# Kernel optimization log

Hardware: AMD Instinct MI355X
Metric: run time of the kernel (lower is better)

The kernel has to match this reference:

```python
import jax, jax.numpy as jnp
import numpy as np

V, D, H, L, F, S, B = 32000, 1024, 16, 6, 4096, 2048, 2
HD = D // H
EPS = 1e-5


def _pos_encoding(seq_len, d_model):
    pos = jnp.arange(seq_len, dtype=jnp.float32)[:, None]
    div = jnp.exp(jnp.arange(0, d_model, 2, dtype=jnp.float32) * (-np.log(10000.0) / d_model))
    pe = jnp.zeros((seq_len, d_model), dtype=jnp.float32)
    pe = pe.at[:, 0::2].set(jnp.sin(pos * div))
    pe = pe.at[:, 1::2].set(jnp.cos(pos * div))
    return pe


def setup_inputs() -> dict:
    key = jax.random.key(0)
    ks = jax.random.split(key, 16)
    tokens = jax.random.randint(ks[0], (B, S), 0, V, dtype=jnp.int64)
    mask = jnp.ones((B, 1, 1, S), dtype=jnp.int32)
    emb = jax.random.normal(ks[1], (V, D), dtype=jnp.float32) * 0.02
    sa = 1.0 / np.sqrt(D)
    sf = 1.0 / np.sqrt(F)
    return {
        "tokens": tokens,
        "mask": mask,
        "emb": emb,
        "Wq": jax.random.normal(ks[2], (L, D, D), dtype=jnp.float32) * sa,
        "bq": jnp.zeros((L, D), dtype=jnp.float32),
        "Wk": jax.random.normal(ks[3], (L, D, D), dtype=jnp.float32) * sa,
        "bk": jnp.zeros((L, D), dtype=jnp.float32),
        "Wv": jax.random.normal(ks[4], (L, D, D), dtype=jnp.float32) * sa,
        "bv": jnp.zeros((L, D), dtype=jnp.float32),
        "Wo": jax.random.normal(ks[5], (L, D, D), dtype=jnp.float32) * sa,
        "bo": jnp.zeros((L, D), dtype=jnp.float32),
        "W1": jax.random.normal(ks[6], (L, D, F), dtype=jnp.float32) * sa,
        "b1": jnp.zeros((L, F), dtype=jnp.float32),
        "W2": jax.random.normal(ks[7], (L, F, D), dtype=jnp.float32) * sf,
        "b2": jnp.zeros((L, D), dtype=jnp.float32),
        "g1": jnp.ones((L, D), dtype=jnp.float32),
        "be1": jnp.zeros((L, D), dtype=jnp.float32),
        "g2": jnp.ones((L, D), dtype=jnp.float32),
        "be2": jnp.zeros((L, D), dtype=jnp.float32),
    }


def _layer_norm(x, g, b):
    m = jnp.mean(x, axis=-1, keepdims=True)
    v = jnp.mean(jnp.square(x - m), axis=-1, keepdims=True)
    return (x - m) * jax.lax.rsqrt(v + EPS) * g + b


def _encoder_stack(x, mask, params):
    scale = 1.0 / np.sqrt(HD)

    def layer(x, p):
        Wq, bq, Wk, bk, Wv, bv, Wo, bo, W1, b1, W2, b2, g1, be1, g2, be2 = p
        b, s, d = x.shape
        q = (x @ Wq + bq).reshape(b, s, H, HD).transpose(0, 2, 1, 3)  # [B,H,S,HD]
        k = (x @ Wk + bk).reshape(b, s, H, HD).transpose(0, 2, 1, 3)
        v = (x @ Wv + bv).reshape(b, s, H, HD).transpose(0, 2, 1, 3)
        scores = jnp.einsum("bhqd,bhkd->bhqk", q, k) * scale
        scores = jnp.where(mask == 0, -1e9, scores)
        attn = jax.nn.softmax(scores, axis=-1)
        ctx = jnp.einsum("bhqk,bhkd->bhqd", attn, v)
        attn_out = ctx.transpose(0, 2, 1, 3).reshape(b, s, d) @ Wo + bo
        x = _layer_norm(x + attn_out, g1, be1)
        ff = jax.nn.relu(x @ W1 + b1) @ W2 + b2
        x = _layer_norm(x + ff, g2, be2)
        return x, None

    x, _ = jax.lax.scan(layer, x, params)
    return x


def reference(tokens, mask, emb, Wq, bq, Wk, bk, Wv, bv, Wo, bo, W1, b1, W2, b2, g1, be1, g2, be2):
    x = emb[tokens] + _pos_encoding(tokens.shape[1], emb.shape[1])[None]
    params = (Wq, bq, Wk, bk, Wv, bv, Wo, bo, W1, b1, W2, b2, g1, be1, g2, be2)
    return _encoder_stack(x, mask, params)
```

## Files before the change

### kernel.cpp

```cpp
#include <hip/hip_runtime.h>
#include <hip/hip_bf16.h>
#include <cstdint>
#include <cstddef>


typedef __bf16 bf16;
typedef __bf16 bf16x2 __attribute__((ext_vector_type(2)));
typedef __bf16 bf16x4 __attribute__((ext_vector_type(4)));
typedef __bf16 bf16x8 __attribute__((ext_vector_type(8)));
typedef float  f32x4  __attribute__((ext_vector_type(4)));

#define MFMA16(a, b, c) __builtin_amdgcn_mfma_f32_16x16x32_bf16((a), (b), (c), 0, 0, 0)

static __device__ __forceinline__ void load_lds16(const void* g, void* l) {
  __builtin_amdgcn_global_load_lds((const __attribute__((address_space(1))) void*)g,
                                   (__attribute__((address_space(3))) void*)l, 16, 0, 0);
}

#define BAR()   __builtin_amdgcn_s_barrier()
#define SCH0()  __builtin_amdgcn_sched_barrier(0)
#define VMCNT8() asm volatile("s_waitcnt vmcnt(8)" ::: "memory")
#define VMCNT0() asm volatile("s_waitcnt vmcnt(0)" ::: "memory")

__global__ __launch_bounds__(256) void embed_kernel(const int* __restrict__ tok,
                                                    const float* __restrict__ emb,
                                                    bf16* __restrict__ xo) {
  const int row = blockIdx.x;
  const int s = row & 2047;
  const int t = tok[row];
  const int d0 = threadIdx.x * 4;
  const float4 e = *(const float4*)&emb[(size_t)t * 1024 + d0];
  const float* ef = (const float*)&e;
  bf16x4 o4;
#pragma unroll
  for (int j = 0; j < 4; ++j) {
    const int d = d0 + j;
    const float div = __expf(-(float)(d & ~1) * 0.00899447301950864f);
    const float arg = (float)s * div;
    const float pe = (d & 1) ? cosf(arg) : sinf(arg);
    o4[j] = (bf16)(ef[j] + pe);
  }
  *(bf16x4*)&xo[(size_t)row * 1024 + d0] = o4;
}

struct TJob { const float* src; bf16* dst; int K; int N; int t0; };
struct TArgs { TJob j[6]; };

__global__ __launch_bounds__(256) void wtrans_kernel(TArgs a) {
  __shared__ float t[32][33];
  const int blk = blockIdx.x;
  const float* src = a.j[0].src; bf16* dst = a.j[0].dst;
  int K = a.j[0].K, N = a.j[0].N, t0 = a.j[0].t0;
#pragma unroll
  for (int q = 1; q < 6; ++q)
    if (blk >= a.j[q].t0) { src = a.j[q].src; dst = a.j[q].dst; K = a.j[q].K; N = a.j[q].N; t0 = a.j[q].t0; }
  const int tj = blk - t0;
  const int tilesK = K >> 5;
  const int tk = (tj % tilesK) << 5;
  const int tn = (tj / tilesK) << 5;
  const int lx = threadIdx.x & 31, ly = threadIdx.x >> 5;
#pragma unroll
  for (int i = 0; i < 4; ++i)
    t[ly + 8 * i][lx] = src[(size_t)(tk + ly + 8 * i) * N + tn + lx];
  __syncthreads();
#pragma unroll
  for (int i = 0; i < 4; ++i)
    dst[(size_t)(tn + ly + 8 * i) * K + tk + lx] = (bf16)t[lx][ly + 8 * i];
}

__global__ __launch_bounds__(256) void vtrans_kernel(const bf16* __restrict__ v,
                                                     bf16* __restrict__ vt) {
  __shared__ bf16 t[64][72];
  const int bh = blockIdx.y;
  const int s0 = blockIdx.x * 64;
  const int tid = threadIdx.x;
#pragma unroll
  for (int it = 0; it < 2; ++it) {
    const int idx = tid + it * 256;
    const int sr = idx >> 3, h8 = (idx & 7) * 8;
    *(bf16x8*)&t[sr][h8] = *(const bf16x8*)&v[((size_t)bh * 2048 + s0 + sr) * 64 + h8];
  }
  __syncthreads();
#pragma unroll
  for (int it = 0; it < 2; ++it) {
    const int idx = tid + it * 256;
    const int hd = idx >> 3, s8 = (idx & 7) * 8;
    bf16x8 o;
#pragma unroll
    for (int j = 0; j < 8; ++j) o[j] = t[s8 + j][hd];
    *(bf16x8*)&vt[((size_t)bh * 64 + hd) * 2048 + s0 + s8] = o;
  }
}

static __device__ __forceinline__ bf16x8 ldsfrag(const bf16* base, int row, int colb) {
  int off = row * 128 + colb;
  off ^= ((off >> 7) & 7) << 4;
  return *(const bf16x8*)((const char*)base + off);
}

static __device__ __forceinline__ void stage_tile(const bf16* __restrict__ Ag,
    const bf16* __restrict__ Bg, int Kstr, int kt, bf16* lA, bf16* lB, int tid) {
  const char* wbaseA = (const char*)lA + ((tid >> 6) << 10);
  const char* wbaseB = (const char*)lB + ((tid >> 6) << 10);
#pragma unroll
  for (int s = 0; s < 4; ++s) {
    const int L = s * 8192 + tid * 16;
    const int off = L ^ (((L >> 7) & 7) << 4);
    load_lds16(Ag + (size_t)(off >> 7) * Kstr + kt * 64 + ((off & 127) >> 1),
               (void*)(wbaseA + s * 8192));
  }
#pragma unroll
  for (int s = 0; s < 4; ++s) {
    const int L = s * 8192 + tid * 16;
    const int off = L ^ (((L >> 7) & 7) << 4);
    load_lds16(Bg + (size_t)(off >> 7) * Kstr + kt * 64 + ((off & 127) >> 1),
               (void*)(wbaseB + s * 8192));
  }
}

static __device__ __forceinline__ void compute_tile(const bf16* lA, const bf16* lB,
    int wm, int wn, int lr, int lg, f32x4 (&acc)[8][4]) {
  bf16x8 bfr[4][2];
#pragma unroll
  for (int n = 0; n < 4; ++n)
#pragma unroll
    for (int kk = 0; kk < 2; ++kk)
      bfr[n][kk] = ldsfrag(lB, wn * 64 + n * 16 + lr, kk * 64 + lg * 16);
#pragma unroll
  for (int m = 0; m < 8; ++m) {
    const bf16x8 a0 = ldsfrag(lA, wm * 128 + m * 16 + lr, lg * 16);
    const bf16x8 a1 = ldsfrag(lA, wm * 128 + m * 16 + lr, 64 + lg * 16);
    __builtin_amdgcn_s_setprio(1);
#pragma unroll
    for (int n = 0; n < 4; ++n) {
      acc[m][n] = MFMA16(a0, bfr[n][0], acc[m][n]);
      acc[m][n] = MFMA16(a1, bfr[n][1], acc[m][n]);
    }
    __builtin_amdgcn_s_setprio(0);
  }
}

template <int EPI>
__global__ __launch_bounds__(512, 2) void gemm256(
    const bf16* __restrict__ A, const bf16* __restrict__ Bt,
    int Kstr, int Kloop, int Nn, int nbx,
    const float* __restrict__ bias0, const float* __restrict__ bias1,
    const float* __restrict__ bias2, bf16* __restrict__ outb,
    float* __restrict__ pout,
    bf16* __restrict__ q_out, bf16* __restrict__ k_out, bf16* __restrict__ v_out) {
  __shared__ __align__(16) bf16 lds[4][16384];
  const int bz = blockIdx.y;
  const bf16* Abase = A + (size_t)bz * Kloop;
  const bf16* Bbase = Bt + (size_t)bz * Kloop;
  const int cpx = gridDim.x >> 3;
  const int wg = (blockIdx.x & 7) * cpx + (blockIdx.x >> 3);
  const int bx = wg % nbx, by = wg / nbx;
  const int tid = threadIdx.x;
  const int lane = tid & 63, wave = tid >> 6;
  const int lr = lane & 15, lg = lane >> 4;
  const int wm = wave >> 2, wn = wave & 3;
  const int m0 = by * 256, n0 = bx * 256;

  const bf16* Ag = Abase + (size_t)m0 * Kstr;
  const bf16* Bg = Bbase + (size_t)n0 * Kstr;
  bf16* LA0 = lds[0]; bf16* LB0 = lds[1];
  bf16* LA1 = lds[2]; bf16* LB1 = lds[3];

  f32x4 acc[8][4] = {};
  const int T = Kloop >> 6;

  stage_tile(Ag, Bg, Kstr, 0, LA0, LB0, tid);
  stage_tile(Ag, Bg, Kstr, 1, LA1, LB1, tid);
  VMCNT8(); BAR(); SCH0();

  for (int t = 0; t + 3 < T; t += 2) {
    compute_tile(LA0, LB0, wm, wn, lr, lg, acc);
    BAR(); SCH0();
    stage_tile(Ag, Bg, Kstr, t + 2, LA0, LB0, tid);
    VMCNT8(); BAR(); SCH0();
    compute_tile(LA1, LB1, wm, wn, lr, lg, acc);
    BAR(); SCH0();
    stage_tile(Ag, Bg, Kstr, t + 3, LA1, LB1, tid);
    VMCNT8(); BAR(); SCH0();
  }
  compute_tile(LA0, LB0, wm, wn, lr, lg, acc);
  VMCNT0(); BAR(); SCH0();
  compute_tile(LA1, LB1, wm, wn, lr, lg, acc);

#pragma unroll
  for (int m = 0; m < 8; ++m)
#pragma unroll
    for (int n = 0; n < 4; ++n)
#pragma unroll
      for (int r = 0; r < 4; ++r) {
        const int row = m0 + wm * 128 + m * 16 + lg * 4 + r;
        const int col = n0 + wn * 64 + n * 16 + lr;
        float val = acc[m][n][r];
        if (EPI == 0) {
          const int which = col >> 10, hc = col & 1023;
          const float* bs = (which == 0) ? bias0 : (which == 1) ? bias1 : bias2;
          bf16* dst = (which == 0) ? q_out : (which == 1) ? k_out : v_out;
          val += bs[hc];
          const int b = row >> 11, s = row & 2047;
          const int h = hc >> 6, hd = hc & 63;
          dst[(((size_t)b * 16 + h) * 2048 + s) * 64 + hd] = (bf16)val;
        } else if (EPI == 1) {
          pout[(size_t)bz * 4096 * 1024 + (size_t)row * 1024 + col] = val;
        } else {
          val += bias0[col];
          outb[(size_t)row * Nn + col] = (bf16)(val > 0.f ? val : 0.f);
        }
      }
}

__global__ __launch_bounds__(256) void gemm_sk(
    const bf16* __restrict__ A, const bf16* __restrict__ Bt,
    int Kstride, int Kloop, int nbx, float* __restrict__ pout) {
  __shared__ __align__(16) bf16 As[128 * 32];
  __shared__ __align__(16) bf16 Bs[128 * 32];
  const int bz = blockIdx.y;
  const bf16* Ab = A + (size_t)bz * Kloop;
  const bf16* Bb = Bt + (size_t)bz * Kloop;
  float* pb = pout + (size_t)bz * 4096 * 1024;
  const int cpx = gridDim.x >> 3;
  const int wg = (blockIdx.x & 7) * cpx + (blockIdx.x >> 3);
  const int bx = wg % nbx, by = wg / nbx;
  const int tid = threadIdx.x;
  const int lane = tid & 63;
  const int wave = tid >> 6;
  const int lr = lane & 15, lg = lane >> 4;
  const int m0 = by * 128;
  const int n0 = bx * 128;
  const int wr = (wave >> 1) * 64, wc = (wave & 1) * 64;

  f32x4 acc[4][4] = {};

  const int idx0 = tid, idx1 = tid + 256;
  const char* gA0 = (const char*)(Ab + (size_t)(m0 + (idx0 >> 2)) * Kstride) + (idx0 & 3) * 16;
  const char* gA1 = (const char*)(Ab + (size_t)(m0 + (idx1 >> 2)) * Kstride) + (idx1 & 3) * 16;
  const char* gB0 = (const char*)(Bb + (size_t)(n0 + (idx0 >> 2)) * Kstride) + (idx0 & 3) * 16;
  const char* gB1 = (const char*)(Bb + (size_t)(n0 + (idx1 >> 2)) * Kstride) + (idx1 & 3) * 16;
  bf16* lA0 = &As[(wave * 64) * 8];
  bf16* lA1 = &As[(256 + wave * 64) * 8];
  bf16* lB0 = &Bs[(wave * 64) * 8];
  bf16* lB1 = &Bs[(256 + wave * 64) * 8];

  const int ksteps = Kloop >> 5;
  for (int kt = 0; kt < ksteps; ++kt) {
    load_lds16(gA0, lA0); load_lds16(gA1, lA1);
    load_lds16(gB0, lB0); load_lds16(gB1, lB1);
    gA0 += 64; gA1 += 64; gB0 += 64; gB1 += 64;
    __syncthreads();
    bf16x8 af[2], bfr[2];
    bf16x8 af2[2], bfr2[2];
#pragma unroll
    for (int i = 0; i < 4; ++i) {
      bf16x8 a = *(const bf16x8*)&As[(wr + i * 16 + lr) * 32 + lg * 8];
      if (i < 2) af[i] = a; else af2[i - 2] = a;
    }
#pragma unroll
    for (int j = 0; j < 4; ++j) {
      bf16x8 b = *(const bf16x8*)&Bs[(wc + j * 16 + lr) * 32 + lg * 8];
      if (j < 2) bfr[j] = b; else bfr2[j - 2] = b;
    }
#pragma unroll
    for (int i = 0; i < 4; ++i)
#pragma unroll
      for (int j = 0; j < 4; ++j) {
        const bf16x8 a = (i < 2) ? af[i & 1] : af2[i & 1];
        const bf16x8 b = (j < 2) ? bfr[j & 1] : bfr2[j & 1];
        acc[i][j] = MFMA16(a, b, acc[i][j]);
      }
    __syncthreads();
  }

#pragma unroll
  for (int i = 0; i < 4; ++i)
#pragma unroll
    for (int j = 0; j < 4; ++j)
#pragma unroll
      for (int r = 0; r < 4; ++r) {
        const int row = m0 + wr + i * 16 + lg * 4 + r;
        const int col = n0 + wc + j * 16 + lr;
        pb[(size_t)row * 1024 + col] = acc[i][j][r];
      }
}

__global__ __launch_bounds__(512) void attn_kernel(const bf16* __restrict__ q,
                                                   const bf16* __restrict__ k,
                                                   const bf16* __restrict__ vt,
                                                   bf16* __restrict__ ctxo) {
  __shared__ __align__(16) bf16 Kl[64][64];
  __shared__ __align__(16) bf16 Vt[64][64];
  __shared__ __align__(16) bf16 Pl[8][16][64];
  const int tid = threadIdx.x;
  const int lane = tid & 63, w = tid >> 6;
  const int lr = lane & 15, lg = lane >> 4;
  const int swz = lr & 7;
  const int bh = blockIdx.y;
  const int q0 = blockIdx.x * 128;

  const bf16* qp = q + ((size_t)bh * 2048 + q0 + w * 16) * 64;
  bf16x8 qf0 = *(const bf16x8*)&qp[lr * 64 + lg * 8];
  bf16x8 qf1 = *(const bf16x8*)&qp[lr * 64 + lg * 8 + 32];
  const float qs = 0.18033688011112042f;
#pragma unroll
  for (int j = 0; j < 8; ++j) {
    qf0[j] = (bf16)((float)qf0[j] * qs);
    qf1[j] = (bf16)((float)qf1[j] * qs);
  }
  bf16x8 ones8;
#pragma unroll
  for (int j = 0; j < 8; ++j) ones8[j] = (bf16)1.0f;

  const bf16* kbase = k + (size_t)bh * 2048 * 64;
  const bf16* vtb = vt + (size_t)bh * 64 * 2048;

  const int sr0 = tid >> 3;
  const int c0 = (tid & 7) * 8;
  const int cs0 = c0 ^ ((sr0 & 7) << 3);

  f32x4 acc[4] = {};
  f32x4 accl = {};
  float mq = -1e30f;

  bf16x8 kr[2], vr[2];
  kr[0] = *(const bf16x8*)&kbase[(size_t)sr0 * 64 + c0];
  vr[0] = *(const bf16x8*)&vtb[(size_t)sr0 * 2048 + c0];

#pragma unroll 2
  for (int c = 0; c < 32; ++c) {
    const int pp = c & 1;
    *(bf16x8*)&Kl[sr0][cs0] = kr[pp];
    *(bf16x8*)&Vt[sr0][cs0] = vr[pp];
    if (c + 1 < 32) {
      const int key0n = (c + 1) * 64;
      kr[pp ^ 1] = *(const bf16x8*)&kbase[(size_t)(key0n + sr0) * 64 + c0];
      vr[pp ^ 1] = *(const bf16x8*)&vtb[(size_t)sr0 * 2048 + key0n + c0];
    }
    __syncthreads();

    f32x4 st[4];
    __builtin_amdgcn_s_setprio(1);
#pragma unroll
    for (int ks = 0; ks < 4; ++ks) {
      const bf16x8 kf0 = *(const bf16x8*)&Kl[ks * 16 + lr][(lg ^ swz) << 3];
      const bf16x8 kf1 = *(const bf16x8*)&Kl[ks * 16 + lr][((lg + 4) ^ swz) << 3];
      f32x4 sa = {};
      sa = MFMA16(kf0, qf0, sa);
      sa = MFMA16(kf1, qf1, sa);
      st[ks] = sa;
    }
    __builtin_amdgcn_s_setprio(0);

    float mx = st[0][0];
#pragma unroll
    for (int ks = 0; ks < 4; ++ks)
#pragma unroll
      for (int r = 0; r < 4; ++r) mx = fmaxf(mx, st[ks][r]);
    mx = fmaxf(mx, __shfl_xor(mx, 16));
    mx = fmaxf(mx, __shfl_xor(mx, 32));
    if (!__all(mx - mq <= 8.0f)) {
      const float resc = exp2f(mq - mx);
      mq = mx;
      float rq[4];
#pragma unroll
      for (int r = 0; r < 4; ++r) rq[r] = __shfl(resc, lg * 4 + r);
#pragma unroll
      for (int r = 0; r < 4; ++r) {
        accl[r] *= rq[r];
#pragma unroll
        for (int jn = 0; jn < 4; ++jn) acc[jn][r] *= rq[r];
      }
    }
#pragma unroll
    for (int ks = 0; ks < 4; ++ks) {
      bf16x4 pk;
#pragma unroll
      for (int r = 0; r < 4; ++r) pk[r] = (bf16)exp2f(st[ks][r] - mq);
      const int col = (((ks * 2 + (lg >> 1)) ^ swz) << 3) + ((lg & 1) << 2);
      *(bf16x4*)&Pl[w][lr][col] = pk;
    }

    const bf16x8 pf0 = *(const bf16x8*)&Pl[w][lr][(lg ^ swz) << 3];
    const bf16x8 pf1 = *(const bf16x8*)&Pl[w][lr][((lg + 4) ^ swz) << 3];
    __builtin_amdgcn_s_setprio(1);
#pragma unroll
    for (int jn = 0; jn < 4; ++jn) {
      const bf16x8 vf0 = *(const bf16x8*)&Vt[jn * 16 + lr][(lg ^ swz) << 3];
      const bf16x8 vf1 = *(const bf16x8*)&Vt[jn * 16 + lr][((lg + 4) ^ swz) << 3];
      acc[jn] = MFMA16(pf0, vf0, acc[jn]);
      acc[jn] = MFMA16(pf1, vf1, acc[jn]);
    }
    accl = MFMA16(pf0, ones8, accl);
    accl = MFMA16(pf1, ones8, accl);
    __builtin_amdgcn_s_setprio(0);
    __syncthreads();
  }

  const int bb = bh >> 4, hh = bh & 15;
#pragma unroll
  for (int r = 0; r < 4; ++r) {
    const float inv = 1.f / accl[r];
    const size_t rowg = (size_t)bb * 2048 + q0 + w * 16 + lg * 4 + r;
#pragma unroll
    for (int jn = 0; jn < 4; ++jn)
      ctxo[rowg * 1024 + hh * 64 + jn * 16 + lr] = (bf16)(acc[jn][r] * inv);
  }
}

template <int NP>
__global__ __launch_bounds__(256) void ln2_kernel(const float* __restrict__ p,
                                                  const bf16* __restrict__ resid,
                                                  const float* __restrict__ bias,
                                                  const float* __restrict__ g,
                                                  const float* __restrict__ be,
                                                  bf16* __restrict__ xo) {
  const int row = blockIdx.x, tid = threadIdx.x;
  const bf16x4 rv = *(const bf16x4*)&resid[(size_t)row * 1024 + tid * 4];
  const float4 bb = ((const float4*)bias)[tid];
  float4 v;
  v.x = bb.x + (float)rv[0];
  v.y = bb.y + (float)rv[1];
  v.z = bb.z + (float)rv[2];
  v.w = bb.w + (float)rv[3];
#pragma unroll
  for (int pl = 0; pl < NP; ++pl) {
    const float4 a = ((const float4*)(p + (size_t)pl * 4096 * 1024 + (size_t)row * 1024))[tid];
    v.x += a.x; v.y += a.y; v.z += a.z; v.w += a.w;
  }
  float s = v.x + v.y + v.z + v.w;
  float s2 = v.x * v.x + v.y * v.y + v.z * v.z + v.w * v.w;
#pragma unroll
  for (int o = 32; o > 0; o >>= 1) { s += __shfl_down(s, o); s2 += __shfl_down(s2, o); }
  __shared__ float red[8];
  if ((tid & 63) == 0) { red[tid >> 6] = s; red[4 + (tid >> 6)] = s2; }
  __syncthreads();
  s = red[0] + red[1] + red[2] + red[3];
  s2 = red[4] + red[5] + red[6] + red[7];
  const float mean = s * (1.f / 1024.f);
  const float var = s2 * (1.f / 1024.f) - mean * mean;
  const float rstd = rsqrtf(var + 1e-5f);
  const float4 gv = ((const float4*)g)[tid];
  const float4 bv = ((const float4*)be)[tid];
  bf16x4 o4;
  o4[0] = (bf16)((v.x - mean) * rstd * gv.x + bv.x);
  o4[1] = (bf16)((v.y - mean) * rstd * gv.y + bv.y);
  o4[2] = (bf16)((v.z - mean) * rstd * gv.z + bv.z);
  o4[3] = (bf16)((v.w - mean) * rstd * gv.w + bv.w);
  *(bf16x4*)&xo[(size_t)row * 1024 + tid * 4] = o4;
}

__global__ __launch_bounds__(256) void to_f32_kernel(const bf16* __restrict__ x,
                                                     float* __restrict__ o) {
  const size_t i = ((size_t)blockIdx.x * 256 + threadIdx.x) * 4;
  const bf16x4 v = *(const bf16x4*)&x[i];
  float4 f;
  f.x = (float)v[0]; f.y = (float)v[1]; f.z = (float)v[2]; f.w = (float)v[3];
  *(float4*)&o[i] = f;
}

extern "C" void kernel_launch(void* const* d_in, const int* in_sizes, int n_in,
                              void* d_out, int out_size, void* d_ws, size_t ws_size,
                              hipStream_t stream) {
  const int* tokens = (const int*)d_in[0];
  const float* emb = (const float*)d_in[2];
  const float* Wq = (const float*)d_in[3];
  const float* bq = (const float*)d_in[4];
  const float* Wk = (const float*)d_in[5];
  const float* bk = (const float*)d_in[6];
  const float* Wv = (const float*)d_in[7];
  const float* bv = (const float*)d_in[8];
  const float* Wo = (const float*)d_in[9];
  const float* bo = (const float*)d_in[10];
  const float* W1 = (const float*)d_in[11];
  const float* b1 = (const float*)d_in[12];
  const float* W2 = (const float*)d_in[13];
  const float* b2 = (const float*)d_in[14];
  const float* g1 = (const float*)d_in[15];
  const float* be1 = (const float*)d_in[16];
  const float* g2 = (const float*)d_in[17];
  const float* be2 = (const float*)d_in[18];

  char* p = (char*)d_ws;
  auto carve = [&](size_t bytes) { char* r = p; p += (bytes + 255) & ~(size_t)255; return r; };
  bf16* wt_qkv = (bf16*)carve((size_t)3072 * 1024 * 2);
  bf16* wt_o   = (bf16*)carve((size_t)1024 * 1024 * 2);
  bf16* wt_1   = (bf16*)carve((size_t)4096 * 1024 * 2);
  bf16* wt_2   = (bf16*)carve((size_t)1024 * 4096 * 2);
  bf16* xb     = (bf16*)carve((size_t)4096 * 1024 * 2);
  bf16* qb     = (bf16*)carve((size_t)4096 * 1024 * 2);
  bf16* kb     = (bf16*)carve((size_t)4096 * 1024 * 2);
  bf16* vb     = (bf16*)carve((size_t)4096 * 1024 * 2);
  bf16* vtb    = (bf16*)carve((size_t)4096 * 1024 * 2);
  bf16* ctxb   = (bf16*)carve((size_t)4096 * 1024 * 2);
  float* pb    = (float*)carve((size_t)4 * 4096 * 1024 * 4);
  bf16* hb     = (bf16*)carve((size_t)4096 * 4096 * 2);

  embed_kernel<<<4096, 256, 0, stream>>>(tokens, emb, xb);

  for (int l = 0; l < 6; ++l) {
    TArgs ta;
    ta.j[0] = { Wq + (size_t)l * 1024 * 1024, wt_qkv,                  1024, 1024, 0 };
    ta.j[1] = { Wk + (size_t)l * 1024 * 1024, wt_qkv + 1024 * 1024,    1024, 1024, 1024 };
    ta.j[2] = { Wv + (size_t)l * 1024 * 1024, wt_qkv + 2 * 1024 * 1024,1024, 1024, 2048 };
    ta.j[3] = { Wo + (size_t)l * 1024 * 1024, wt_o,                    1024, 1024, 3072 };
    ta.j[4] = { W1 + (size_t)l * 1024 * 4096, wt_1,                    1024, 4096, 4096 };
    ta.j[5] = { W2 + (size_t)l * 4096 * 1024, wt_2,                    4096, 1024, 8192 };
    wtrans_kernel<<<12288, 256, 0, stream>>>(ta);

    gemm256<0><<<192, 512, 0, stream>>>(xb, wt_qkv, 1024, 1024, 3072, 12,
        bq + (size_t)l * 1024, bk + (size_t)l * 1024, bv + (size_t)l * 1024,
        nullptr, nullptr, qb, kb, vb);

    vtrans_kernel<<<dim3(32, 32), 256, 0, stream>>>(vb, vtb);

    attn_kernel<<<dim3(16, 32), 512, 0, stream>>>(qb, kb, vtb, ctxb);

    gemm_sk<<<dim3(256, 2), 256, 0, stream>>>(ctxb, wt_o, 1024, 512, 8, pb);
    ln2_kernel<2><<<4096, 256, 0, stream>>>(pb, xb, bo + (size_t)l * 1024,
        g1 + (size_t)l * 1024, be1 + (size_t)l * 1024, xb);

    gemm256<2><<<256, 512, 0, stream>>>(xb, wt_1, 1024, 1024, 4096, 16,
        b1 + (size_t)l * 4096, nullptr, nullptr, hb,
        nullptr, nullptr, nullptr, nullptr);

    gemm256<1><<<dim3(64, 4), 512, 0, stream>>>(hb, wt_2, 4096, 1024, 1024, 4,
        nullptr, nullptr, nullptr, nullptr, pb,
        nullptr, nullptr, nullptr);
    ln2_kernel<4><<<4096, 256, 0, stream>>>(pb, xb, b2 + (size_t)l * 1024,
        g2 + (size_t)l * 1024, be2 + (size_t)l * 1024, xb);
  }

  to_f32_kernel<<<4096, 256, 0, stream>>>(xb, (float*)d_out);
}
```

Before: 1.443 ms.

## Replace split-K output GEMMs with 128x128 full-K GEMM fusing bias and residual

The Wo and W2 projections previously used split-K: partial fp32 sums were written to a 4-plane buffer and reduced in the layernorm kernel. They now go through a new pipelined 128x128-tile GEMM that runs the full K loop, with swizzled LDS staging and double buffering. Its epilogue adds bias and residual and writes a single fp32 output, so the layernorm only normalizes. This removes the partial-sum write and read traffic, at the cost of fewer, longer blocks: 256 blocks each running the whole K, which is 4096 for W2.

After: 1.429 ms. Within noise of the previous version (-1.0%).

```diff
diff --git a/kernel.cpp b/kernel.cpp
--- a/kernel.cpp
+++ b/kernel.cpp
@@ -146,12 +146,8 @@
     int Kstr, int Kloop, int Nn, int nbx,
     const float* __restrict__ bias0, const float* __restrict__ bias1,
     const float* __restrict__ bias2, bf16* __restrict__ outb,
-    float* __restrict__ pout,
     bf16* __restrict__ q_out, bf16* __restrict__ k_out, bf16* __restrict__ v_out) {
   __shared__ __align__(16) bf16 lds[4][16384];
-  const int bz = blockIdx.y;
-  const bf16* Abase = A + (size_t)bz * Kloop;
-  const bf16* Bbase = Bt + (size_t)bz * Kloop;
   const int cpx = gridDim.x >> 3;
   const int wg = (blockIdx.x & 7) * cpx + (blockIdx.x >> 3);
   const int bx = wg % nbx, by = wg / nbx;
@@ -161,8 +157,8 @@
   const int wm = wave >> 2, wn = wave & 3;
   const int m0 = by * 256, n0 = bx * 256;
 
-  const bf16* Ag = Abase + (size_t)m0 * Kstr;
-  const bf16* Bg = Bbase + (size_t)n0 * Kstr;
+  const bf16* Ag = A + (size_t)m0 * Kstr;
+  const bf16* Bg = Bt + (size_t)n0 * Kstr;
   bf16* LA0 = lds[0]; bf16* LB0 = lds[1];
   bf16* LA1 = lds[2]; bf16* LB1 = lds[3];
 
@@ -204,8 +200,6 @@
           const int b = row >> 11, s = row & 2047;
           const int h = hc >> 6, hd = hc & 63;
           dst[(((size_t)b * 16 + h) * 2048 + s) * 64 + hd] = (bf16)val;
-        } else if (EPI == 1) {
-          pout[(size_t)bz * 4096 * 1024 + (size_t)row * 1024 + col] = val;
         } else {
           val += bias0[col];
           outb[(size_t)row * Nn + col] = (bf16)(val > 0.f ? val : 0.f);
@@ -213,76 +207,99 @@
       }
 }
 
-__global__ __launch_bounds__(256) void gemm_sk(
-    const bf16* __restrict__ A, const bf16* __restrict__ Bt,
-    int Kstride, int Kloop, int nbx, float* __restrict__ pout) {
-  __shared__ __align__(16) bf16 As[128 * 32];
-  __shared__ __align__(16) bf16 Bs[128 * 32];
-  const int bz = blockIdx.y;
-  const bf16* Ab = A + (size_t)bz * Kloop;
-  const bf16* Bb = Bt + (size_t)bz * Kloop;
-  float* pb = pout + (size_t)bz * 4096 * 1024;
+static __device__ __forceinline__ void stage128(const bf16* __restrict__ Ag,
+    const bf16* __restrict__ Bg, int Kstr, int kt, bf16* lA, bf16* lB, int tid) {
+  const char* dA = (const char*)lA + ((tid >> 6) << 10);
+  const char* dB = (const char*)lB + ((tid >> 6) << 10);
+#pragma unroll
+  for (int s = 0; s < 4; ++s) {
+    const int L = s * 4096 + tid * 16;
+    const int off = L ^ (((L >> 7) & 7) << 4);
+    load_lds16(Ag + (size_t)(off >> 7) * Kstr + kt * 64 + ((off & 127) >> 1),
+               (void*)(dA + s * 4096));
+  }
+#pragma unroll
+  for (int s = 0; s < 4; ++s) {
+    const int L = s * 4096 + tid * 16;
+    const int off = L ^ (((L >> 7) & 7) << 4);
+    load_lds16(Bg + (size_t)(off >> 7) * Kstr + kt * 64 + ((off & 127) >> 1),
+               (void*)(dB + s * 4096));
+  }
+}
+
+static __device__ __forceinline__ void compute128(const bf16* lA, const bf16* lB,
+    int wm, int wn, int lr, int lg, f32x4 (&acc)[4][4]) {
+  bf16x8 bfr[4][2];
+#pragma unroll
+  for (int n = 0; n < 4; ++n)
+#pragma unroll
+    for (int kk = 0; kk < 2; ++kk)
+      bfr[n][kk] = ldsfrag(lB, wn * 64 + n * 16 + lr, kk * 64 + lg * 16);
+#pragma unroll
+  for (int m = 0; m < 4; ++m) {
+    const bf16x8 a0 = ldsfrag(lA, wm * 64 + m * 16 + lr, lg * 16);
+    const bf16x8 a1 = ldsfrag(lA, wm * 64 + m * 16 + lr, 64 + lg * 16);
+    __builtin_amdgcn_s_setprio(1);
+#pragma unroll
+    for (int n = 0; n < 4; ++n) {
+      acc[m][n] = MFMA16(a0, bfr[n][0], acc[m][n]);
+      acc[m][n] = MFMA16(a1, bfr[n][1], acc[m][n]);
+    }
+    __builtin_amdgcn_s_setprio(0);
+  }
+}
+
+__global__ __launch_bounds__(256, 2) void gemm128p(
+    const bf16* __restrict__ A, const bf16* __restrict__ Bt, int Kk,
+    const float* __restrict__ bias, const bf16* __restrict__ resid,
+    float* __restrict__ outf) {
+  __shared__ __align__(16) bf16 lds[4][8192];
   const int cpx = gridDim.x >> 3;
   const int wg = (blockIdx.x & 7) * cpx + (blockIdx.x >> 3);
-  const int bx = wg % nbx, by = wg / nbx;
+  const int bx = wg & 7, by = wg >> 3;
   const int tid = threadIdx.x;
-  const int lane = tid & 63;
-  const int wave = tid >> 6;
+  const int lane = tid & 63, wave = tid >> 6;
   const int lr = lane & 15, lg = lane >> 4;
-  const int m0 = by * 128;
-  const int n0 = bx * 128;
-  const int wr = (wave >> 1) * 64, wc = (wave & 1) * 64;
+  const int wm = wave >> 1, wn = wave & 1;
+  const int m0 = by * 128, n0 = bx * 128;
+
+  const bf16* Ag = A + (size_t)m0 * Kk;
+  const bf16* Bg = Bt + (size_t)n0 * Kk;
+  bf16* LA0 = lds[0]; bf16* LB0 = lds[1];
+  bf16* LA1 = lds[2]; bf16* LB1 = lds[3];
 
   f32x4 acc[4][4] = {};
-
-  const int idx0 = tid, idx1 = tid + 256;
-  const char* gA0 = (const char*)(Ab + (size_t)(m0 + (idx0 >> 2)) * Kstride) + (idx0 & 3) * 16;
-  const char* gA1 = (const char*)(Ab + (size_t)(m0 + (idx1 >> 2)) * Kstride) + (idx1 & 3) * 16;
-  const char* gB0 = (const char*)(Bb + (size_t)(n0 + (idx0 >> 2)) * Kstride) + (idx0 & 3) * 16;
-  const char* gB1 = (const char*)(Bb + (size_t)(n0 + (idx1 >> 2)) * Kstride) + (idx1 & 3) * 16;
-  bf16* lA0 = &As[(wave * 64) * 8];
-  bf16* lA1 = &As[(256 + wave * 64) * 8];
-  bf16* lB0 = &Bs[(wave * 64) * 8];
-  bf16* lB1 = &Bs[(256 + wave * 64) * 8];
-
-  const int ksteps = Kloop >> 5;
-  for (int kt = 0; kt < ksteps; ++kt) {
-    load_lds16(gA0, lA0); load_lds16(gA1, lA1);
-    load_lds16(gB0, lB0); load_lds16(gB1, lB1);
-    gA0 += 64; gA1 += 64; gB0 += 64; gB1 += 64;
-    __syncthreads();
-    bf16x8 af[2], bfr[2];
-    bf16x8 af2[2], bfr2[2];
-#pragma unroll
-    for (int i = 0; i < 4; ++i) {
-      bf16x8 a = *(const bf16x8*)&As[(wr + i * 16 + lr) * 32 + lg * 8];
-      if (i < 2) af[i] = a; else af2[i - 2] = a;
-    }
-#pragma unroll
-    for (int j = 0; j < 4; ++j) {
-      bf16x8 b = *(const bf16x8*)&Bs[(wc + j * 16 + lr) * 32 + lg * 8];
-      if (j < 2) bfr[j] = b; else bfr2[j - 2] = b;
-    }
-#pragma unroll
-    for (int i = 0; i < 4; ++i)
-#pragma unroll
-      for (int j = 0; j < 4; ++j) {
-        const bf16x8 a = (i < 2) ? af[i & 1] : af2[i & 1];
-        const bf16x8 b = (j < 2) ? bfr[j & 1] : bfr2[j & 1];
-        acc[i][j] = MFMA16(a, b, acc[i][j]);
-      }
-    __syncthreads();
-  }
-
-#pragma unroll
-  for (int i = 0; i < 4; ++i)
-#pragma unroll
-    for (int j = 0; j < 4; ++j)
+  const int T = Kk >> 6;
+
+  stage128(Ag, Bg, Kk, 0, LA0, LB0, tid);
+  stage128(Ag, Bg, Kk, 1, LA1, LB1, tid);
+  VMCNT8(); BAR(); SCH0();
+
+  for (int t = 0; t + 3 < T; t += 2) {
+    compute128(LA0, LB0, wm, wn, lr, lg, acc);
+    BAR(); SCH0();
+    stage128(Ag, Bg, Kk, t + 2, LA0, LB0, tid);
+    VMCNT8(); BAR(); SCH0();
+    compute128(LA1, LB1, wm, wn, lr, lg, acc);
+    BAR(); SCH0();
+    stage128(Ag, Bg, Kk, t + 3, LA1, LB1, tid);
+    VMCNT8(); BAR(); SCH0();
+  }
+  compute128(LA0, LB0, wm, wn, lr, lg, acc);
+  VMCNT0(); BAR(); SCH0();
+  compute128(LA1, LB1, wm, wn, lr, lg, acc);
+
+#pragma unroll
+  for (int m = 0; m < 4; ++m)
+#pragma unroll
+    for (int n = 0; n < 4; ++n)
 #pragma unroll
       for (int r = 0; r < 4; ++r) {
-        const int row = m0 + wr + i * 16 + lg * 4 + r;
-        const int col = n0 + wc + j * 16 + lr;
-        pb[(size_t)row * 1024 + col] = acc[i][j][r];
+        const int row = m0 + wm * 64 + m * 16 + lg * 4 + r;
+        const int col = n0 + wn * 64 + n * 16 + lr;
+        const float val = acc[m][n][r] + bias[col]
+                        + (float)resid[(size_t)row * 1024 + col];
+        outf[(size_t)row * 1024 + col] = val;
       }
 }
 
@@ -409,26 +426,12 @@
   }
 }
 
-template <int NP>
-__global__ __launch_bounds__(256) void ln2_kernel(const float* __restrict__ p,
-                                                  const bf16* __restrict__ resid,
-                                                  const float* __restrict__ bias,
-                                                  const float* __restrict__ g,
-                                                  const float* __restrict__ be,
-                                                  bf16* __restrict__ xo) {
+__global__ __launch_bounds__(256) void ln_kernel(const float* __restrict__ y,
+                                                 const float* __restrict__ g,
+                                                 const float* __restrict__ be,
+                                                 bf16* __restrict__ xo) {
   const int row = blockIdx.x, tid = threadIdx.x;
-  const bf16x4 rv = *(const bf16x4*)&resid[(size_t)row * 1024 + tid * 4];
-  const float4 bb = ((const float4*)bias)[tid];
-  float4 v;
-  v.x = bb.x + (float)rv[0];
-  v.y = bb.y + (float)rv[1];
-  v.z = bb.z + (float)rv[2];
-  v.w = bb.w + (float)rv[3];
-#pragma unroll
-  for (int pl = 0; pl < NP; ++pl) {
-    const float4 a = ((const float4*)(p + (size_t)pl * 4096 * 1024 + (size_t)row * 1024))[tid];
-    v.x += a.x; v.y += a.y; v.z += a.z; v.w += a.w;
-  }
+  const float4 v = ((const float4*)(y + (size_t)row * 1024))[tid];
   float s = v.x + v.y + v.z + v.w;
   float s2 = v.x * v.x + v.y * v.y + v.z * v.z + v.w * v.w;
 #pragma unroll
@@ -494,7 +497,7 @@
   bf16* vb     = (bf16*)carve((size_t)4096 * 1024 * 2);
   bf16* vtb    = (bf16*)carve((size_t)4096 * 1024 * 2);
   bf16* ctxb   = (bf16*)carve((size_t)4096 * 1024 * 2);
-  float* pb    = (float*)carve((size_t)4 * 4096 * 1024 * 4);
+  float* yb    = (float*)carve((size_t)4096 * 1024 * 4);
   bf16* hb     = (bf16*)carve((size_t)4096 * 4096 * 2);
 
   embed_kernel<<<4096, 256, 0, stream>>>(tokens, emb, xb);
@@ -511,25 +514,25 @@
 
     gemm256<0><<<192, 512, 0, stream>>>(xb, wt_qkv, 1024, 1024, 3072, 12,
         bq + (size_t)l * 1024, bk + (size_t)l * 1024, bv + (size_t)l * 1024,
-        nullptr, nullptr, qb, kb, vb);
+        nullptr, qb, kb, vb);
 
     vtrans_kernel<<<dim3(32, 32), 256, 0, stream>>>(vb, vtb);
 
     attn_kernel<<<dim3(16, 32), 512, 0, stream>>>(qb, kb, vtb, ctxb);
 
-    gemm_sk<<<dim3(256, 2), 256, 0, stream>>>(ctxb, wt_o, 1024, 512, 8, pb);
-    ln2_kernel<2><<<4096, 256, 0, stream>>>(pb, xb, bo + (size_t)l * 1024,
-        g1 + (size_t)l * 1024, be1 + (size_t)l * 1024, xb);
+    gemm128p<<<256, 256, 0, stream>>>(ctxb, wt_o, 1024,
+        bo + (size_t)l * 1024, xb, yb);
+    ln_kernel<<<4096, 256, 0, stream>>>(yb, g1 + (size_t)l * 1024,
+        be1 + (size_t)l * 1024, xb);
 
     gemm256<2><<<256, 512, 0, stream>>>(xb, wt_1, 1024, 1024, 4096, 16,
         b1 + (size_t)l * 4096, nullptr, nullptr, hb,
-        nullptr, nullptr, nullptr, nullptr);
-
-    gemm256<1><<<dim3(64, 4), 512, 0, stream>>>(hb, wt_2, 4096, 1024, 1024, 4,
-        nullptr, nullptr, nullptr, nullptr, pb,
         nullptr, nullptr, nullptr);
-    ln2_kernel<4><<<4096, 256, 0, stream>>>(pb, xb, b2 + (size_t)l * 1024,
-        g2 + (size_t)l * 1024, be2 + (size_t)l * 1024, xb);
+
+    gemm128p<<<256, 256, 0, stream>>>(hb, wt_2, 4096,
+        b2 + (size_t)l * 1024, xb, yb);
+    ln_kernel<<<4096, 256, 0, stream>>>(yb, g2 + (size_t)l * 1024,
+        be2 + (size_t)l * 1024, xb);
   }
 
   to_f32_kernel<<<4096, 256, 0, stream>>>(xb, (float*)d_out);
```
